# Kernel tuning notes

Measured on AMD Instinct MI355X. Metric: run time of the kernel, lower is better.

Reference implementation:

```python
import jax, jax.numpy as jnp
import numpy as np

N, D, K = 500000, 128, 16

def _glorot(key, shape):
    lim = np.sqrt(6.0 / (shape[0] + shape[-1]))
    return jax.random.uniform(key, shape, jnp.float32, -lim, lim)

def setup_inputs() -> dict:
    key = jax.random.key(0)
    k1, k2, kV, kW, kU = jax.random.split(key, 5)
    x1 = jax.random.normal(k1, (N, D), jnp.float32)
    x2 = jax.random.normal(k2, (1, D), jnp.float32)
    V = _glorot(kV, (K, 2 * D))
    W = _glorot(kW, (K, D, D))
    b = jnp.zeros((K,), jnp.float32)
    U = _glorot(kU, (K, 1))
    return {"x1": x1, "x2": x2, "V": V, "W": W, "b": b, "U": U}

def reference(x1, x2, V, W, b, U):
    # V-term: concat([x1, tile(x2)]) @ V[i]^T, vectorized over K by splitting V.
    d = x1.shape[1]
    v_term = x1 @ V[:, :d].T + x2 @ V[:, d:].T            # (N,K) + (1,K)
    # W-term: (x1 @ W[i]) @ x2^T for each i == x1 @ (W @ x2)^T, vectorized.
    wx2 = jnp.einsum('kde,e->kd', W, x2[0])               # (K,D)
    w_term = x1 @ wx2.T                                   # (N,K)
    out = jax.nn.relu(v_term + w_term + b)                # (N,K)
    return out @ U                                        # (N,1)
```

## Files before the change

### kernel.cpp

```cpp
#include <hip/hip_runtime.h>
#include <hip/hip_bf16.h>


#define D 128
#define KK 16

typedef __attribute__((ext_vector_type(8))) short bf16x8;
typedef __attribute__((ext_vector_type(4))) float f32x4;

__device__ __forceinline__ unsigned short f2bf(float f) {
    unsigned u = __float_as_uint(f);
    unsigned t = u + 0x7fffu + ((u >> 16) & 1u);
    return (unsigned short)(t >> 16);
}
__device__ __forceinline__ float bf2f(unsigned short s) {
    return __uint_as_float(((unsigned)s) << 16);
}

__global__ __launch_bounds__(256) void ntn_prep(const float* __restrict__ x2,
                                                const float* __restrict__ V,
                                                const float* __restrict__ W,
                                                const float* __restrict__ b,
                                                unsigned short* __restrict__ bh,
                                                unsigned short* __restrict__ bl,
                                                float* __restrict__ c) {
    const int gtid = blockIdx.x * 256 + threadIdx.x;
    const int wave = gtid >> 6;
    const int lane = gtid & 63;
    if (wave >= KK * D + KK) return;

    float p;
    if (wave < KK * D) {
        const int k = wave >> 7, d = wave & (D - 1);
        const float* Wr = W + ((size_t)(k * D + d)) * D;
        p = Wr[lane] * x2[lane] + Wr[lane + 64] * x2[lane + 64];
    } else {
        const int k = wave - KK * D;
        const float* Vr = V + (size_t)k * 2 * D + D;
        p = Vr[lane] * x2[lane] + Vr[lane + 64] * x2[lane + 64];
    }
#pragma unroll
    for (int m = 32; m; m >>= 1) p += __shfl_xor(p, m);

    if (lane == 0) {
        if (wave < KK * D) {
            const int k = wave >> 7, d = wave & (D - 1);
            float Mv = V[(size_t)k * 2 * D + d] + p;
            unsigned short hb = f2bf(Mv);
            unsigned short lb = f2bf(Mv - bf2f(hb));
            const int kb = d >> 5, kk = d & 31;
            const int fl = k | ((kk >> 3) << 4);
            const int idx = kb * 512 + fl * 8 + (kk & 7);
            bh[idx] = hb;
            bl[idx] = lb;
        } else {
            const int k = wave - KK * D;
            c[k] = p + b[k];
        }
    }
}

__global__ __launch_bounds__(256, 4) void ntn_main(const float* __restrict__ x1,
                                                   const unsigned short* __restrict__ bhp,
                                                   const unsigned short* __restrict__ blp,
                                                   const float* __restrict__ cp,
                                                   const float* __restrict__ Up,
                                                   float* __restrict__ out,
                                                   int NT, int TW) {
    const int t = threadIdx.x;
    const int l = t & 63;
    const int gw = blockIdx.x * 4 + (t >> 6);

    bf16x8 Bh[4], Bl[4];
#pragma unroll
    for (int kb = 0; kb < 4; ++kb) {
        Bh[kb] = *(const bf16x8*)(bhp + kb * 512 + l * 8);
        Bl[kb] = *(const bf16x8*)(blp + kb * 512 + l * 8);
    }
    const int m = l & 15;
    const int q = l >> 4;
    const float cl = cp[m];
    const float ul = Up[m];

    int i = gw;
    if (i >= NT) return;

    float4 cur[8];
    {
        const float4* p = (const float4*)(x1 + ((size_t)i * 16 + m) * D + q * 8);
#pragma unroll
        for (int kb = 0; kb < 4; ++kb) { cur[2 * kb] = p[kb * 8]; cur[2 * kb + 1] = p[kb * 8 + 1]; }
    }

    while (true) {
        const int nx = i + TW;
        const bool has = nx < NT;
        float4 nb[8];
        if (has) {
            const float4* p = (const float4*)(x1 + ((size_t)nx * 16 + m) * D + q * 8);
#pragma unroll
            for (int kb = 0; kb < 4; ++kb) { nb[2 * kb] = p[kb * 8]; nb[2 * kb + 1] = p[kb * 8 + 1]; }
        }

        f32x4 accA = {0.f, 0.f, 0.f, 0.f};
        f32x4 accB = {0.f, 0.f, 0.f, 0.f};
#pragma unroll
        for (int kb = 0; kb < 4; ++kb) {
            const float f[8] = {cur[2 * kb].x,     cur[2 * kb].y,     cur[2 * kb].z,     cur[2 * kb].w,
                                cur[2 * kb + 1].x, cur[2 * kb + 1].y, cur[2 * kb + 1].z, cur[2 * kb + 1].w};
            bf16x8 ah;
#pragma unroll
            for (int j = 0; j < 8; ++j) ah[j] = (short)f2bf(f[j]);
            accA = __builtin_amdgcn_mfma_f32_16x16x32_bf16(ah, Bh[kb], accA, 0, 0, 0);
            accB = __builtin_amdgcn_mfma_f32_16x16x32_bf16(ah, Bl[kb], accB, 0, 0, 0);
        }

        float4 v;
        {
            float vv[4];
#pragma unroll
            for (int r = 0; r < 4; ++r) {
                float s = accA[r] + accB[r] + cl;
                vv[r] = ul * fmaxf(s, 0.f);
                vv[r] += __shfl_xor(vv[r], 1);
                vv[r] += __shfl_xor(vv[r], 2);
                vv[r] += __shfl_xor(vv[r], 4);
                vv[r] += __shfl_xor(vv[r], 8);
            }
            v = make_float4(vv[0], vv[1], vv[2], vv[3]);
        }
        if (m == 0) *(float4*)(out + (size_t)i * 16 + q * 4) = v;

        if (!has) break;
#pragma unroll
        for (int j = 0; j < 8; ++j) cur[j] = nb[j];
        i = nx;
    }
}

extern "C" void kernel_launch(void* const* d_in, const int* in_sizes, int n_in,
                              void* d_out, int out_size, void* d_ws, size_t ws_size,
                              hipStream_t stream) {
    const float* x1 = (const float*)d_in[0];
    const float* x2 = (const float*)d_in[1];
    const float* V  = (const float*)d_in[2];
    const float* W  = (const float*)d_in[3];
    const float* b  = (const float*)d_in[4];
    const float* U  = (const float*)d_in[5];
    float* out = (float*)d_out;

    unsigned short* bh = (unsigned short*)d_ws;
    unsigned short* bl = bh + KK * D;
    float* c = (float*)(bl + KK * D);

    const int N = in_sizes[0] / D;
    const int NT = N >> 4;

    ntn_prep<<<516, 256, 0, stream>>>(x2, V, W, b, bh, bl, c);

    const int blocks = 1024;
    ntn_main<<<blocks, 256, 0, stream>>>(x1, bh, bl, c, U, out, NT, blocks * 4);
}
```

Measured before the change: 349.3 us.

## Coalesce x1 loads and stage bf16 tiles through swizzled LDS per wave

Each wave now loads its 16-row tile of x1 with fully contiguous float4 reads, converts to bf16 with packed intrinsics, and writes to a per-wave XOR-swizzled LDS buffer. MFMA operands are then read back from LDS in the layout the instruction expects. Each wave also processes a contiguous chunk of tiles instead of a grid-strided sequence. This targets uncoalesced strided global reads and the per-element scalar bf16 conversion, at the cost of extra LDS traffic and relying on wave-local ordering with no explicit barrier.

```diff
diff --git a/kernel.cpp b/kernel.cpp
--- a/kernel.cpp
+++ b/kernel.cpp
@@ -60,16 +60,26 @@
     }
 }
 
+__device__ __forceinline__ uint2 pack4(const float4& v) {
+    union { __hip_bfloat162 h; unsigned u; } a, b;
+    a.h = __float22bfloat162_rn(make_float2(v.x, v.y));
+    b.h = __float22bfloat162_rn(make_float2(v.z, v.w));
+    uint2 r; r.x = a.u; r.y = b.u; return r;
+}
+
 __global__ __launch_bounds__(256, 4) void ntn_main(const float* __restrict__ x1,
                                                    const unsigned short* __restrict__ bhp,
                                                    const unsigned short* __restrict__ blp,
                                                    const float* __restrict__ cp,
                                                    const float* __restrict__ Up,
                                                    float* __restrict__ out,
-                                                   int NT, int TW) {
+                                                   int NT, int C) {
+    __shared__ unsigned char lds[4 * 4096];
+
     const int t = threadIdx.x;
     const int l = t & 63;
     const int gw = blockIdx.x * 4 + (t >> 6);
+    unsigned char* const L = lds + (t >> 6) * 4096;
 
     bf16x8 Bh[4], Bl[4];
 #pragma unroll
@@ -82,40 +92,49 @@
     const float cl = cp[m];
     const float ul = Up[m];
 
-    int i = gw;
-    if (i >= NT) return;
+    const int start = gw * C;
+    if (start >= NT) return;
+    const int end = (start + C < NT) ? start + C : NT;
 
-    float4 cur[8];
+    const int wr_r0 = (l >> 5);
+    const int wr_cb = (l & 31) * 8;
+    int rd_off[4];
+#pragma unroll
+    for (int kb = 0; kb < 4; ++kb)
+        rd_off[kb] = m * 256 + ((kb * 64 + q * 16) ^ ((m & 7) * 16));
+
+    const float4* const f4 = (const float4*)x1;
+
     {
-        const float4* p = (const float4*)(x1 + ((size_t)i * 16 + m) * D + q * 8);
+        float4 g[8];
+        const size_t base = (size_t)start * 512 + l;
 #pragma unroll
-        for (int kb = 0; kb < 4; ++kb) { cur[2 * kb] = p[kb * 8]; cur[2 * kb + 1] = p[kb * 8 + 1]; }
+        for (int i = 0; i < 8; ++i) g[i] = f4[base + i * 64];
+#pragma unroll
+        for (int i = 0; i < 8; ++i) {
+            const int r = wr_r0 + 2 * i;
+            *(uint2*)(L + r * 256 + (wr_cb ^ ((r & 7) * 16))) = pack4(g[i]);
+        }
     }
 
-    while (true) {
-        const int nx = i + TW;
-        const bool has = nx < NT;
-        float4 nb[8];
+    for (int i = start; i < end; ++i) {
+        const bool has = (i + 1 < end);
+        float4 g2[8];
         if (has) {
-            const float4* p = (const float4*)(x1 + ((size_t)nx * 16 + m) * D + q * 8);
+            const size_t base = (size_t)(i + 1) * 512 + l;
 #pragma unroll
-            for (int kb = 0; kb < 4; ++kb) { nb[2 * kb] = p[kb * 8]; nb[2 * kb + 1] = p[kb * 8 + 1]; }
+            for (int j = 0; j < 8; ++j) g2[j] = f4[base + j * 64];
         }
 
         f32x4 accA = {0.f, 0.f, 0.f, 0.f};
         f32x4 accB = {0.f, 0.f, 0.f, 0.f};
 #pragma unroll
         for (int kb = 0; kb < 4; ++kb) {
-            const float f[8] = {cur[2 * kb].x,     cur[2 * kb].y,     cur[2 * kb].z,     cur[2 * kb].w,
-                                cur[2 * kb + 1].x, cur[2 * kb + 1].y, cur[2 * kb + 1].z, cur[2 * kb + 1].w};
-            bf16x8 ah;
-#pragma unroll
-            for (int j = 0; j < 8; ++j) ah[j] = (short)f2bf(f[j]);
+            bf16x8 ah = *(const bf16x8*)(L + rd_off[kb]);
             accA = __builtin_amdgcn_mfma_f32_16x16x32_bf16(ah, Bh[kb], accA, 0, 0, 0);
             accB = __builtin_amdgcn_mfma_f32_16x16x32_bf16(ah, Bl[kb], accB, 0, 0, 0);
         }
 
-        float4 v;
         {
             float vv[4];
 #pragma unroll
@@ -127,14 +146,18 @@
                 vv[r] += __shfl_xor(vv[r], 4);
                 vv[r] += __shfl_xor(vv[r], 8);
             }
-            v = make_float4(vv[0], vv[1], vv[2], vv[3]);
+            if (m == 0)
+                *(float4*)(out + (size_t)i * 16 + q * 4) =
+                    make_float4(vv[0], vv[1], vv[2], vv[3]);
         }
-        if (m == 0) *(float4*)(out + (size_t)i * 16 + q * 4) = v;
 
-        if (!has) break;
+        if (has) {
 #pragma unroll
-        for (int j = 0; j < 8; ++j) cur[j] = nb[j];
-        i = nx;
+            for (int j = 0; j < 8; ++j) {
+                const int r = wr_r0 + 2 * j;
+                *(uint2*)(L + r * 256 + (wr_cb ^ ((r & 7) * 16))) = pack4(g2[j]);
+            }
+        }
     }
 }
 
@@ -158,6 +181,7 @@
 
     ntn_prep<<<516, 256, 0, stream>>>(x2, V, W, b, bh, bl, c);
 
-    const int blocks = 1024;
-    ntn_main<<<blocks, 256, 0, stream>>>(x1, bh, bl, c, U, out, NT, blocks * 4);
+    const int waves = 1024 * 4;
+    const int C = (NT + waves - 1) / waves;
+    ntn_main<<<1024, 256, 0, stream>>>(x1, bh, bl, c, U, out, NT, C);
 }
```

Result: slower. 360.8 us (+3.3%).
